# Optimization experiments

Measured on AMD Instinct MI355X. Metric: run time of the kernel, lower is better.

The kernel has to match this reference:

```python
import jax, jax.numpy as jnp
import numpy as np

DIM = 1024
HEADS = 16
HEAD_DIM = DIM // HEADS
B, N = 2, 2048


def setup_inputs() -> dict:
    key = jax.random.key(0)
    k1, k2, k3, k4 = jax.random.split(key, 4)
    x = jax.random.normal(k1, (B, N, DIM), dtype=jnp.float32)
    # torch Linear weights: shape (out_features, in_features), y = x @ W.T + b
    w_qkv = jax.random.normal(k2, (3 * DIM, DIM), dtype=jnp.float32) * (DIM ** -0.5)
    w_proj = jax.random.normal(k3, (DIM, DIM), dtype=jnp.float32) * (DIM ** -0.5)
    b_proj = jax.random.normal(k4, (DIM,), dtype=jnp.float32) * 0.01
    return {"x": x, "w_qkv": w_qkv, "w_proj": w_proj, "b_proj": b_proj}


def reference(x, w_qkv, w_proj, b_proj):
    Bb, Nn, D = x.shape
    scale = HEAD_DIM ** -0.5
    qkv = x @ w_qkv.T                                # [B, N, 3D]
    qkv = qkv.reshape(Bb, Nn, 3, HEADS, HEAD_DIM)
    qkv = jnp.transpose(qkv, (2, 0, 3, 1, 4))        # [3, B, H, N, hd]
    q, k, v = qkv[0], qkv[1], qkv[2]
    attn = jnp.einsum('bhqd,bhkd->bhqk', q, k) * scale
    attn = jax.nn.softmax(attn, axis=-1)
    out = jnp.einsum('bhqk,bhkd->bhqd', attn, v)     # [B, H, N, hd]
    out = jnp.transpose(out, (0, 2, 1, 3)).reshape(Bb, Nn, D)
    return out @ w_proj.T + b_proj
```

## Files before the change

kernel.cpp:

```cpp
#include <hip/hip_runtime.h>
#include <cstdint>
#include <cstddef>

using u16 = unsigned short;
using u32 = uint32_t;
using f32x4  = __attribute__((ext_vector_type(4))) float;
using bf16x8 = __attribute__((ext_vector_type(8))) __bf16;
using s16x4  = __attribute__((ext_vector_type(4))) short;

#define D_MODEL 1024
#define N_HEADS 16
#define HD      64
#define SEQ     2048
#define QKV_LD  3072
#define K2SCALE 0.18033688011112042f

__device__ __forceinline__ u16 f2b(float f) {
  union { float f; u32 u; } v; v.f = f;
  u32 r = 0x7FFFu + ((v.u >> 16) & 1u);
  return (u16)((v.u + r) >> 16);
}

__device__ __forceinline__ u32 pkbf16(float a, float b) {
  return (u32)f2b(a) | ((u32)f2b(b) << 16);
}

#define MFMA16(A, B, C) __builtin_amdgcn_mfma_f32_16x16x16bf16_1k(A, B, C, 0, 0, 0)

__device__ __forceinline__ void gld16(const u16* g, u16* l) {
  __builtin_amdgcn_global_load_lds(
      (const __attribute__((address_space(1))) void*)g,
      (__attribute__((address_space(3))) void*)l, 16, 0, 0);
}

__global__ void cast_bf16(const float* __restrict__ src, u16* __restrict__ dst) {
  int i = blockIdx.x * blockDim.x + threadIdx.x;
  float4 f = ((const float4*)src)[i];
  ushort4 o;
  o.x = f2b(f.x); o.y = f2b(f.y); o.z = f2b(f.z); o.w = f2b(f.w);
  ((ushort4*)dst)[i] = o;
}

template<int OUTMODE, int MT>
__launch_bounds__(256, 3)
__global__ void gemm_nt(const u16* __restrict__ A, const u16* __restrict__ B,
                        u16* __restrict__ Ob, float* __restrict__ Of,
                        const float* __restrict__ bias, int N, int K) {
  __shared__ __attribute__((aligned(16))) u16 sA[MT * 32];
  __shared__ __attribute__((aligned(16))) u16 sB[128 * 32];

  const int tid  = threadIdx.x;
  const int lane = tid & 63;
  const int w    = tid >> 6;
  const int qd   = lane >> 4;
  const int ln   = lane & 15;
  constexpr int MI = MT / 32;
  const int wm   = (w >> 1) * (MT / 2);
  const int wn   = (w & 1) * 64;
  const int m0   = blockIdx.y * MT;
  const int n0   = blockIdx.x * 128;

  f32x4 acc[MI][4] = {};

  for (int k0 = 0; k0 < K; k0 += 32) {
    __syncthreads();
    #pragma unroll
    for (int c = 0; c < MT / 64; ++c) {
      int sbase = w * MT + c * 64;
      int s = sbase + lane;
      int row = s >> 2, col = (s & 3) * 8;
      gld16(A + (size_t)(m0 + row) * K + k0 + col, &sA[sbase * 8]);
    }
    #pragma unroll
    for (int c = 0; c < 2; ++c) {
      int sbase = w * 128 + c * 64;
      int s = sbase + lane;
      int row = s >> 2, col = (s & 3) * 8;
      gld16(B + (size_t)(n0 + row) * K + k0 + col, &sB[sbase * 8]);
    }
    __syncthreads();

    bf16x8 af[MI], bfm[4];
    #pragma unroll
    for (int i = 0; i < MI; ++i)
      af[i] = *(const bf16x8*)&sA[(wm + i * 16 + ln) * 32 + qd * 8];
    #pragma unroll
    for (int j = 0; j < 4; ++j)
      bfm[j] = *(const bf16x8*)&sB[(wn + j * 16 + ln) * 32 + qd * 8];
    #pragma unroll
    for (int i = 0; i < MI; ++i)
      #pragma unroll
      for (int j = 0; j < 4; ++j)
        acc[i][j] = __builtin_amdgcn_mfma_f32_16x16x32_bf16(af[i], bfm[j], acc[i][j], 0, 0, 0);
  }

  #pragma unroll
  for (int i = 0; i < MI; ++i) {
    #pragma unroll
    for (int j = 0; j < 4; ++j) {
      #pragma unroll
      for (int r = 0; r < 4; ++r) {
        int row = m0 + wm + i * 16 + qd * 4 + r;
        int col = n0 + wn + j * 16 + ln;
        float v = acc[i][j][r];
        if (OUTMODE == 0) {
          if (col < D_MODEL) v *= K2SCALE;
          Ob[(size_t)row * N + col] = f2b(v);
        } else {
          Of[(size_t)row * N + col] = v + bias[col];
        }
      }
    }
  }
}

__launch_bounds__(256, 2)
__global__ void attn_kernel(const u16* __restrict__ qkv, u16* __restrict__ outb) {
  __shared__ __attribute__((aligned(16))) u16 sK[2][2][128 * 32];
  __shared__ __attribute__((aligned(16))) u32 sVT[2][64 * 68];

  const int tid  = threadIdx.x;
  const int lane = tid & 63;
  const int w    = tid >> 6;
  const int qd   = lane >> 4;
  const int ln   = lane & 15;
  const int qp   = blockIdx.x;
  const int h    = blockIdx.y & 15;
  const int b    = blockIdx.y >> 4;
  const size_t tokbase = (size_t)b * SEQ;
  const int q0   = qp * 128;
  const int qoff = h * HD;
  const int koff = D_MODEL + h * HD;
  const int voff = 2 * D_MODEL + h * HD;

  bf16x8 aq[2][2];
  #pragma unroll
  for (int c2 = 0; c2 < 2; ++c2)
    #pragma unroll
    for (int hf = 0; hf < 2; ++hf)
      aq[c2][hf] = *(const bf16x8*)(qkv + (tokbase + q0 + c2 * 64 + w * 16 + ln) * QKV_LD
                                    + qoff + hf * 32 + qd * 8);

  auto stageK = [&](int kt, int buf) {
    #pragma unroll
    for (int hf = 0; hf < 2; ++hf)
      #pragma unroll
      for (int c = 0; c < 2; ++c) {
        int sbase = w * 128 + c * 64;
        int s = sbase + lane;
        int row = s >> 2, col = (s & 3) * 8;
        gld16(qkv + (tokbase + kt * 128 + row) * QKV_LD + koff + hf * 32 + col,
              &sK[buf][hf][sbase * 8]);
      }
  };
  auto loadV = [&](int kt, uint4* va, uint4* vb) {
    #pragma unroll
    for (int it = 0; it < 2; ++it) {
      int j = it * 256 + tid;
      int tp = j & 63, d0 = (j >> 6) * 8;
      const u16* g0 = qkv + (tokbase + kt * 128 + tp * 2) * QKV_LD + voff + d0;
      va[it] = *(const uint4*)g0;
      vb[it] = *(const uint4*)(g0 + QKV_LD);
    }
  };
  auto writeV = [&](int buf, const uint4* va, const uint4* vb) {
    #pragma unroll
    for (int it = 0; it < 2; ++it) {
      int j = it * 256 + tid;
      int tp = j & 63, d0 = (j >> 6) * 8;
      const u32* a  = (const u32*)&va[it];
      const u32* bb = (const u32*)&vb[it];
      #pragma unroll
      for (int e = 0; e < 4; ++e) {
        sVT[buf][(d0 + 2 * e    ) * 68 + tp] = __builtin_amdgcn_perm(bb[e], a[e], 0x05040100u);
        sVT[buf][(d0 + 2 * e + 1) * 68 + tp] = __builtin_amdgcn_perm(bb[e], a[e], 0x07060302u);
      }
    }
  };

  stageK(0, 0);
  uint4 va[2], vb[2];
  loadV(0, va, vb);
  writeV(0, va, vb);
  loadV(1, va, vb);

  f32x4 accOT[2][4] = {};
  float psum[2] = {0.f, 0.f};

  for (int kt = 0; kt < 16; ++kt) {
    const int cur = kt & 1, nxt = cur ^ 1;
    __syncthreads();
    if (kt < 15) { stageK(kt + 1, nxt); writeV(nxt, va, vb); }
    if (kt < 14) { loadV(kt + 2, va, vb); }

    #pragma unroll
    for (int cb = 0; cb < 8; ++cb) {
      bf16x8 ak0 = *(const bf16x8*)&sK[cur][0][(cb * 16 + ln) * 32 + qd * 8];
      bf16x8 ak1 = *(const bf16x8*)&sK[cur][1][(cb * 16 + ln) * 32 + qd * 8];
      f32x4 st[2];
      #pragma unroll
      for (int c2 = 0; c2 < 2; ++c2) {
        f32x4 z = {0.f, 0.f, 0.f, 0.f};
        f32x4 t = __builtin_amdgcn_mfma_f32_16x16x32_bf16(ak0, aq[c2][0], z, 0, 0, 0);
        st[c2]  = __builtin_amdgcn_mfma_f32_16x16x32_bf16(ak1, aq[c2][1], t, 0, 0, 0);
      }
      s16x4 pf[2];
      #pragma unroll
      for (int c2 = 0; c2 < 2; ++c2) {
        float p0 = __builtin_amdgcn_exp2f(st[c2][0]);
        float p1 = __builtin_amdgcn_exp2f(st[c2][1]);
        float p2 = __builtin_amdgcn_exp2f(st[c2][2]);
        float p3 = __builtin_amdgcn_exp2f(st[c2][3]);
        psum[c2] += (p0 + p1) + (p2 + p3);
        union { u32 d[2]; s16x4 v; } pk;
        pk.d[0] = pkbf16(p0, p1);
        pk.d[1] = pkbf16(p2, p3);
        pf[c2] = pk.v;
      }
      #pragma unroll
      for (int ob = 0; ob < 4; ++ob) {
        s16x4 vf = *(const s16x4*)&sVT[cur][(ob * 16 + ln) * 68 + cb * 8 + qd * 2];
        accOT[0][ob] = MFMA16(vf, pf[0], accOT[0][ob]);
        accOT[1][ob] = MFMA16(vf, pf[1], accOT[1][ob]);
      }
    }
  }

  #pragma unroll
  for (int c2 = 0; c2 < 2; ++c2) {
    float s = psum[c2];
    s += __shfl_xor(s, 16, 64);
    s += __shfl_xor(s, 32, 64);
    psum[c2] = 1.0f / s;
  }

  u16* sOut = (u16*)&sK[0][0][0];
  __syncthreads();
  #pragma unroll
  for (int c2 = 0; c2 < 2; ++c2)
    #pragma unroll
    for (int ob = 0; ob < 4; ++ob) {
      u32 lo = pkbf16(accOT[c2][ob][0] * psum[c2], accOT[c2][ob][1] * psum[c2]);
      u32 hi = pkbf16(accOT[c2][ob][2] * psum[c2], accOT[c2][ob][3] * psum[c2]);
      ((u32*)sOut)[(c2 * 64 + w * 16 + ln) * 36 + ob * 8 + qd * 2    ] = lo;
      ((u32*)sOut)[(c2 * 64 + w * 16 + ln) * 36 + ob * 8 + qd * 2 + 1] = hi;
    }
  __syncthreads();
  #pragma unroll
  for (int it = 0; it < 4; ++it) {
    int idx = it * 256 + tid;
    int token = idx >> 3, chunk = idx & 7;
    uint4 v = *(const uint4*)&sOut[token * 72 + chunk * 8];
    *(uint4*)&outb[(tokbase + q0 + token) * D_MODEL + h * HD + chunk * 8] = v;
  }
}

extern "C" void kernel_launch(void* const* d_in, const int* in_sizes, int n_in,
                              void* d_out, int out_size, void* d_ws, size_t ws_size,
                              hipStream_t stream) {
  const float* x      = (const float*)d_in[0];
  const float* w_qkv  = (const float*)d_in[1];
  const float* w_proj = (const float*)d_in[2];
  const float* b_proj = (const float*)d_in[3];
  float* out = (float*)d_out;

  u16* ws     = (u16*)d_ws;
  u16* xb     = ws;
  u16* wqkvb  = xb    + (size_t)4096 * 1024;
  u16* wprojb = wqkvb + (size_t)3072 * 1024;
  u16* qkvb   = wprojb + (size_t)1024 * 1024;
  u16* attnb  = qkvb  + (size_t)4096 * 3072;

  cast_bf16<<<4096, 256, 0, stream>>>(x,      xb);
  cast_bf16<<<3072, 256, 0, stream>>>(w_qkv,  wqkvb);
  cast_bf16<<<1024, 256, 0, stream>>>(w_proj, wprojb);

  gemm_nt<0, 128><<<dim3(24, 32), 256, 0, stream>>>(xb, wqkvb, qkvb, nullptr, nullptr, 3072, 1024);

  attn_kernel<<<dim3(16, 32), 256, 0, stream>>>(qkvb, attnb);

  gemm_nt<1, 64><<<dim3(8, 64), 256, 0, stream>>>(attnb, wprojb, nullptr, out, b_proj, 1024, 1024);
}
```

Before: 200.3 us.

## Double-buffer GEMM LDS, swizzle V transpose, fuse cast kernels

The GEMM kernel now double-buffers its LDS tiles so the next k-slice's global-to-LDS loads overlap the current MFMAs. The attention kernel replaces the padded V^T layout with an XOR swizzle to avoid bank conflicts with less LDS. The three fp32-to-bf16 casts are merged into one launch. Together these raise LDS use in the GEMM, which may reduce occupancy.

```diff
diff --git a/kernel.cpp b/kernel.cpp
--- a/kernel.cpp
+++ b/kernel.cpp
@@ -33,9 +33,15 @@
       (__attribute__((address_space(3))) void*)l, 16, 0, 0);
 }
 
-__global__ void cast_bf16(const float* __restrict__ src, u16* __restrict__ dst) {
+__global__ void cast3_bf16(const float* __restrict__ x, const float* __restrict__ wq,
+                           const float* __restrict__ wp, u16* __restrict__ dst) {
   int i = blockIdx.x * blockDim.x + threadIdx.x;
-  float4 f = ((const float4*)src)[i];
+  const float* src;
+  int off;
+  if (blockIdx.x < 4096)      { src = x;  off = 0; }
+  else if (blockIdx.x < 7168) { src = wq; off = 4096 * 256; }
+  else                        { src = wp; off = 7168 * 256; }
+  float4 f = ((const float4*)src)[i - off];
   ushort4 o;
   o.x = f2b(f.x); o.y = f2b(f.y); o.z = f2b(f.z); o.w = f2b(f.w);
   ((ushort4*)dst)[i] = o;
@@ -46,8 +52,8 @@
 __global__ void gemm_nt(const u16* __restrict__ A, const u16* __restrict__ B,
                         u16* __restrict__ Ob, float* __restrict__ Of,
                         const float* __restrict__ bias, int N, int K) {
-  __shared__ __attribute__((aligned(16))) u16 sA[MT * 32];
-  __shared__ __attribute__((aligned(16))) u16 sB[128 * 32];
+  __shared__ __attribute__((aligned(16))) u16 sA[2][MT * 32];
+  __shared__ __attribute__((aligned(16))) u16 sB[2][128 * 32];
 
   const int tid  = threadIdx.x;
   const int lane = tid & 63;
@@ -60,33 +66,40 @@
   const int m0   = blockIdx.y * MT;
   const int n0   = blockIdx.x * 128;
 
-  f32x4 acc[MI][4] = {};
-
-  for (int k0 = 0; k0 < K; k0 += 32) {
-    __syncthreads();
+  auto stage = [&](int kk, int buf) {
+    int k0 = kk * 32;
     #pragma unroll
     for (int c = 0; c < MT / 64; ++c) {
       int sbase = w * MT + c * 64;
       int s = sbase + lane;
       int row = s >> 2, col = (s & 3) * 8;
-      gld16(A + (size_t)(m0 + row) * K + k0 + col, &sA[sbase * 8]);
+      gld16(A + (size_t)(m0 + row) * K + k0 + col, &sA[buf][sbase * 8]);
     }
     #pragma unroll
     for (int c = 0; c < 2; ++c) {
       int sbase = w * 128 + c * 64;
       int s = sbase + lane;
       int row = s >> 2, col = (s & 3) * 8;
-      gld16(B + (size_t)(n0 + row) * K + k0 + col, &sB[sbase * 8]);
-    }
+      gld16(B + (size_t)(n0 + row) * K + k0 + col, &sB[buf][sbase * 8]);
+    }
+  };
+
+  f32x4 acc[MI][4] = {};
+  const int NK = K >> 5;
+  stage(0, 0);
+
+  for (int kk = 0; kk < NK; ++kk) {
+    const int cur = kk & 1;
     __syncthreads();
+    if (kk + 1 < NK) stage(kk + 1, cur ^ 1);
 
     bf16x8 af[MI], bfm[4];
     #pragma unroll
     for (int i = 0; i < MI; ++i)
-      af[i] = *(const bf16x8*)&sA[(wm + i * 16 + ln) * 32 + qd * 8];
+      af[i] = *(const bf16x8*)&sA[cur][(wm + i * 16 + ln) * 32 + qd * 8];
     #pragma unroll
     for (int j = 0; j < 4; ++j)
-      bfm[j] = *(const bf16x8*)&sB[(wn + j * 16 + ln) * 32 + qd * 8];
+      bfm[j] = *(const bf16x8*)&sB[cur][(wn + j * 16 + ln) * 32 + qd * 8];
     #pragma unroll
     for (int i = 0; i < MI; ++i)
       #pragma unroll
@@ -117,7 +130,7 @@
 __launch_bounds__(256, 2)
 __global__ void attn_kernel(const u16* __restrict__ qkv, u16* __restrict__ outb) {
   __shared__ __attribute__((aligned(16))) u16 sK[2][2][128 * 32];
-  __shared__ __attribute__((aligned(16))) u32 sVT[2][64 * 68];
+  __shared__ __attribute__((aligned(16))) u32 sVT[2][64 * 64];
 
   const int tid  = threadIdx.x;
   const int lane = tid & 63;
@@ -172,8 +185,10 @@
       const u32* bb = (const u32*)&vb[it];
       #pragma unroll
       for (int e = 0; e < 4; ++e) {
-        sVT[buf][(d0 + 2 * e    ) * 68 + tp] = __builtin_amdgcn_perm(bb[e], a[e], 0x05040100u);
-        sVT[buf][(d0 + 2 * e + 1) * 68 + tp] = __builtin_amdgcn_perm(bb[e], a[e], 0x07060302u);
+        sVT[buf][(d0 + 2 * e    ) * 64 + (tp ^ (e << 4)      )] =
+            __builtin_amdgcn_perm(bb[e], a[e], 0x05040100u);
+        sVT[buf][(d0 + 2 * e + 1) * 64 + (tp ^ (e << 4) ^ 8  )] =
+            __builtin_amdgcn_perm(bb[e], a[e], 0x07060302u);
       }
     }
   };
@@ -186,6 +201,7 @@
 
   f32x4 accOT[2][4] = {};
   float psum[2] = {0.f, 0.f};
+  const int tsw = (ln & 7) << 3;
 
   for (int kt = 0; kt < 16; ++kt) {
     const int cur = kt & 1, nxt = cur ^ 1;
@@ -219,7 +235,8 @@
       }
       #pragma unroll
       for (int ob = 0; ob < 4; ++ob) {
-        s16x4 vf = *(const s16x4*)&sVT[cur][(ob * 16 + ln) * 68 + cb * 8 + qd * 2];
+        s16x4 vf = *(const s16x4*)&sVT[cur][(ob * 16 + ln) * 64
+                                           + ((cb * 8 + qd * 2) ^ tsw)];
         accOT[0][ob] = MFMA16(vf, pf[0], accOT[0][ob]);
         accOT[1][ob] = MFMA16(vf, pf[1], accOT[1][ob]);
       }
@@ -271,9 +288,7 @@
   u16* qkvb   = wprojb + (size_t)1024 * 1024;
   u16* attnb  = qkvb  + (size_t)4096 * 3072;
 
-  cast_bf16<<<4096, 256, 0, stream>>>(x,      xb);
-  cast_bf16<<<3072, 256, 0, stream>>>(w_qkv,  wqkvb);
-  cast_bf16<<<1024, 256, 0, stream>>>(w_proj, wprojb);
+  cast3_bf16<<<8192, 256, 0, stream>>>(x, w_qkv, w_proj, xb);
 
   gemm_nt<0, 128><<<dim3(24, 32), 256, 0, stream>>>(xb, wqkvb, qkvb, nullptr, nullptr, 3072, 1024);
 
```

Result: no change. 197.6 us (-1.4%).
